# Kernel optimization log

Hardware: AMD Instinct MI355X
Metric: run time of the kernel (lower is better)

## Reference

```python
import jax, jax.numpy as jnp
import numpy as np

NEG = -1e9  # finite stand-in for log(0); keeps logsumexp/vjp NaN-free


def _hsmm_forward_loglik(log_B, log_pi, log_A, log_D):
    """Explicit-duration HSMM forward recursion in log-space for one sequence.

    log_B: (T, K) emission log-probs per state
    log_pi: (K,) initial state logits (log-normalized)
    log_A: (K, K) semi-Markov transition logits (NEG on diagonal, rows log-normalized)
    log_D: (K, Dmax) duration logits (rows log-normalized); column d <-> duration d+1
    Returns scalar log-likelihood log p(x_{1:T}).
    """
    T, K = log_B.shape
    Dmax = log_D.shape[1]
    # cB[t, j] = sum of emission log-probs of state j over first t steps; cB[0] = 0
    cB = jnp.concatenate([jnp.zeros((1, K), log_B.dtype), jnp.cumsum(log_B, axis=0)], axis=0)  # (T+1, K)
    log_Dt = log_D.T  # (Dmax, K), row d = duration d+1

    buf0 = jnp.full((Dmax, K), NEG, log_B.dtype)     # rolling buffer of start[t'] - cB[t']
    alpha0 = jnp.full((K,), NEG, log_B.dtype)

    def step(carry, t):
        buf, alpha_prev = carry
        # start[t, j]: log-prob a new segment starts at time t in state j
        trans = jax.scipy.special.logsumexp(alpha_prev[:, None] + log_A, axis=0)  # (K,)
        start = jnp.where(t == 0, log_pi, trans)
        buf = jnp.roll(buf, 1, axis=0).at[0].set(start - cB[t])
        # alpha[t, j] = cB[t+1, j] + lse_d ( start[t-d] - cB[t-d] + log_D[j, d] )
        alpha = cB[t + 1] + jax.scipy.special.logsumexp(buf + log_Dt, axis=0)  # (K,)
        return (buf, alpha), None
    (_, alpha_T), _ = jax.lax.scan(step, (buf0, alpha0), jnp.arange(T))
    return jax.scipy.special.logsumexp(alpha_T)


def setup_inputs() -> dict:
    key = jax.random.key(0)
    kB, kpi, kA, kD = jax.random.split(key, 4)
    B, T, K, Dmax = 32, 8192, 128, 128
    # emission log-probs (abstract emission pdf delegated to subclass -> model as input)
    log_B = jax.random.normal(kB, (B, T, K), dtype=jnp.float32) - 2.0
    log_pi = jax.nn.log_softmax(jax.random.normal(kpi, (K,), dtype=jnp.float32))
    # SEMI constraint: no self-transitions (diagonal = -inf), rows log-normalized
    A_raw = jax.random.normal(kA, (K, K), dtype=jnp.float32)
    A_raw = jnp.where(jnp.eye(K, dtype=bool), NEG, A_raw)
    log_A = jax.nn.log_softmax(A_raw, axis=1)
    log_D = jax.nn.log_softmax(jax.random.normal(kD, (K, Dmax), dtype=jnp.float32), axis=1)
    return {"log_B": log_B, "log_pi": log_pi, "log_A": log_A, "log_D": log_D}


def reference(log_B, log_pi, log_A, log_D):
    # Batched HSMM forward algorithm: per-sequence log-likelihoods, shape (B,)
    return jax.vmap(_hsmm_forward_loglik, in_axes=(0, None, None, None))(log_B, log_pi, log_A, log_D)
```

## Files before the change

kernel.cpp:

```cpp
#include <hip/hip_runtime.h>


typedef float f32x2 __attribute__((ext_vector_type(2)));

#define T_LEN 8192
#define KST   128
#define NTHR  512
#define SROW  160

__device__ __forceinline__ void barrier_nodrain() {
  asm volatile("s_waitcnt lgkmcnt(0)\n\ts_barrier" ::: "memory");
}

template <int CTRL>
__device__ __forceinline__ float dpp_mov(float x) {
  int y = __builtin_amdgcn_update_dpp(0, __builtin_bit_cast(int, x),
                                      CTRL, 0xF, 0xF, true);
  return __builtin_bit_cast(float, y);
}
template <int CTRL>
__device__ __forceinline__ f32x2 dpp_addv(f32x2 x) {
  f32x2 y;
  y.x = dpp_mov<CTRL>(x.x);
  y.y = dpp_mov<CTRL>(x.y);
  return x + y;
}

__device__ __forceinline__ void pk_fma(f32x2& d, f32x2 a, f32x2 b) {
  asm("v_pk_fma_f32 %0, %1, %2, %0" : "+v"(d) : "v"(a), "v"(b));
}
__device__ __forceinline__ void pk_fma_blo(f32x2& d, f32x2 a, f32x2 b) {
  asm("v_pk_fma_f32 %0, %1, %2, %0 op_sel:[0,0,0] op_sel_hi:[1,0,1]"
      : "+v"(d) : "v"(a), "v"(b));
}
__device__ __forceinline__ void pk_fma_bhi(f32x2& d, f32x2 a, f32x2 b) {
  asm("v_pk_fma_f32 %0, %1, %2, %0 op_sel:[0,1,0] op_sel_hi:[1,1,1]"
      : "+v"(d) : "v"(a), "v"(b));
}
__device__ __forceinline__ f32x2 pk_mul(f32x2 a, f32x2 b) {
  f32x2 d;
  asm("v_pk_mul_f32 %0, %1, %2" : "=v"(d) : "v"(a), "v"(b));
  return d;
}

template <int U>
__device__ __forceinline__ void step_body(
    int t0, int cc, int w, int L, int sel, int c2, int cc16,
    const float* __restrict__ pB0, const float* __restrict__ pB1,
    f32x2 (&qq)[16], const f32x2 (&Apl)[8], const f32x2 (&Aph)[8],
    f32x2 (&ee)[16], float (&lb0)[16], float (&lb1)[16],
    int& off,
    f32x2& psi, f32x2& invpsi, f32x2& exq, float& Ctot, f32x2& skeep,
    f32x2 expD0p, f32x2 pexpp, int swaddr,
    float* s_flat, float* m_sc, const float* ep_flat)
{
  const int t = t0 + U;
  const f32x2 expB = exq;

  int tn = t + 16; tn = (tn < T_LEN) ? tn : (T_LEN - 1);
  lb0[U] = pB0[(size_t)tn * KST];
  lb1[U] = pB1[(size_t)tn * KST];

  if (U == 15) {
    int rn = (t0 + 16 - cc16) & 127;
    int cl = (c2 + 4 * ((rn >> 4) & 7)) & 127;
    off = rn * 512 + cl * 4;
  } else {
    off = (off + 512) & 0xFFFF;
  }
  const f32x2 ne =
      *reinterpret_cast<const f32x2*>(reinterpret_cast<const char*>(ep_flat) + off);

  float Mp = m_sc[U & 1];

  const float* sp = s_flat + (U & 1) * SROW + 20 * cc;
  const float4 v0 = *(const float4*)(sp + 0),  v1 = *(const float4*)(sp + 4);
  const float4 v2 = *(const float4*)(sp + 8),  v3 = *(const float4*)(sp + 12);

  f32x2 da = pk_mul(qq[0], ee[(0 - U) & 15]);
  f32x2 db = pk_mul(qq[1], ee[(1 - U) & 15]);
#pragma unroll
  for (int k = 2; k < 16; k += 2) {
    pk_fma(da, qq[k],     ee[(k - U) & 15]);
    pk_fma(db, qq[k + 1], ee[(k + 1 - U) & 15]);
  }
  f32x2 dp = da + db;

  Mp = fminf(fmaxf(Mp, 1e-30f), 1e30f);
  const float rMp = __builtin_amdgcn_rcpf(Mp);
  Ctot += __logf(Mp);
  psi = pk_mul(psi, pk_mul(expB, f32x2{rMp, rMp}));

  f32x2 ma = {0.0f, 0.0f}, mb = {0.0f, 0.0f};
  pk_fma_blo(ma, Apl[0], f32x2{v0.x, v0.y});  pk_fma_bhi(mb, Aph[0], f32x2{v0.x, v0.y});
  pk_fma_blo(ma, Apl[1], f32x2{v0.z, v0.w});  pk_fma_bhi(mb, Aph[1], f32x2{v0.z, v0.w});
  pk_fma_blo(ma, Apl[2], f32x2{v1.x, v1.y});  pk_fma_bhi(mb, Aph[2], f32x2{v1.x, v1.y});
  pk_fma_blo(ma, Apl[3], f32x2{v1.z, v1.w});  pk_fma_bhi(mb, Aph[3], f32x2{v1.z, v1.w});
  pk_fma_blo(ma, Apl[4], f32x2{v2.x, v2.y});  pk_fma_bhi(mb, Aph[4], f32x2{v2.x, v2.y});
  pk_fma_blo(ma, Apl[5], f32x2{v2.z, v2.w});  pk_fma_bhi(mb, Aph[5], f32x2{v2.z, v2.w});
  pk_fma_blo(ma, Apl[6], f32x2{v3.x, v3.y});  pk_fma_bhi(mb, Aph[6], f32x2{v3.x, v3.y});
  pk_fma_blo(ma, Apl[7], f32x2{v3.z, v3.w});  pk_fma_bhi(mb, Aph[7], f32x2{v3.z, v3.w});
  f32x2 mp = ma + mb;

  dp = dpp_addv<0xB1>(dp); dp = dpp_addv<0x4E>(dp); dp = dpp_addv<0x141>(dp);
  mp = dpp_addv<0xB1>(mp); mp = dpp_addv<0x4E>(mp); mp = dpp_addv<0x141>(mp);

  f32x2 Qins = pk_mul(mp, invpsi);
  if (U == 0) { if (t0 == 0) Qins = pexpp; }
  f32x2 sacc = dp;
  pk_fma(sacc, Qins, expD0p);
  const f32x2 s = pk_mul(sacc, psi);

  exq.x = __expf(lb0[(U + 1) & 15]);
  exq.y = __expf(lb1[(U + 1) & 15]);

  if (sel == cc) qq[U] = Qins;

  if (w == 0) {
    float sm = fmaxf(s.x, s.y);
    sm = fmaxf(sm, dpp_mov<0x140>(sm));
    sm = fmaxf(sm, dpp_mov<0x142>(sm));
    sm = fmaxf(sm, dpp_mov<0x143>(sm));
    if (L == 63) m_sc[(U + 1) & 1] = sm;
  }

  if (cc == 0)
    *reinterpret_cast<f32x2*>(s_flat + ((U + 1) & 1) * SROW + swaddr) = s;

  ee[(15 - U) & 15] = ne;

  if (U == 15) {
#pragma unroll
    for (int k = 0; k < 16; ++k) qq[k] = pk_mul(qq[k], psi);
    psi = f32x2{1.0f, 1.0f};
  }
  invpsi.x = __builtin_amdgcn_rcpf(psi.x);
  invpsi.y = __builtin_amdgcn_rcpf(psi.y);

  skeep = s;
  barrier_nodrain();
}

__global__ __launch_bounds__(NTHR, 1) void hsmm_fwd_kernel(
    const float* __restrict__ logB_all,
    const float* __restrict__ logpi,
    const float* __restrict__ logA,
    const float* __restrict__ logD,
    float* __restrict__ out)
{
  const int tid = threadIdx.x;
  const int L   = tid & 63;
  const int w   = tid >> 6;
  const int cc  = L & 7;
  const int g   = L >> 3;
  const int j0  = 8 * w + g;
  const int j1  = j0 + 64;
  const int b   = blockIdx.x;
  const float* __restrict__ pB0 = logB_all + (size_t)b * T_LEN * KST + j0;
  const float* __restrict__ pB1 = pB0 + 64;

  __shared__ __align__(16) float epair[128 * 128];
  __shared__ __align__(16) float s_lds[2 * SROW];
  __shared__ float m_sc[2];
  __shared__ float fin[8];

  for (int idx = tid; idx < 128 * 128; idx += NTHR) {
    int d = idx >> 7, r = idx & 127;
    int j = r >> 1, hb = r & 1;
    int col = ((2 * j + 4 * ((d >> 4) & 7)) & 127) + hb;
    epair[(d << 7) + col] = (d == 0) ? 0.0f : __expf(logD[(j + 64 * hb) * 128 + d]);
  }
  if (tid < 2 * SROW) s_lds[tid] = 0.0f;
  if (tid < 2) m_sc[tid] = 1.0f;

  f32x2 Apl[8], Aph[8];
#pragma unroll
  for (int k = 0; k < 8; ++k) {
    int m = 8 * cc + k;
    Apl[k].x = __expf(logA[m * KST + j0]);
    Apl[k].y = __expf(logA[m * KST + j1]);
    Aph[k].x = __expf(logA[(m + 64) * KST + j0]);
    Aph[k].y = __expf(logA[(m + 64) * KST + j1]);
  }
  const f32x2 expD0p = {__expf(logD[j0 * 128]), __expf(logD[j1 * 128])};
  const f32x2 pexpp  = {__expf(logpi[j0]), __expf(logpi[j1])};
  const int   swaddr = 20 * w + 2 * g;
  const int   c2     = 16 * w + 2 * g;
  const int   cc16   = 16 * cc;

  f32x2 qq[16];
#pragma unroll
  for (int k = 0; k < 16; ++k) qq[k] = f32x2{0.0f, 0.0f};

  __syncthreads();

  f32x2 ee[16];
#pragma unroll
  for (int k = 0; k < 16; ++k) {
    int rA = (-(cc16 + k)) & 127;
    int cl = (c2 + 4 * ((rA >> 4) & 7)) & 127;
    ee[k] = *reinterpret_cast<const f32x2*>(&epair[(rA << 7) + cl]);
  }

  int off;
  {
    int r0 = (-cc16) & 127;
    int cl = (c2 + 4 * ((r0 >> 4) & 7)) & 127;
    off = r0 * 512 + cl * 4;
  }

  float lb0[16], lb1[16];
#pragma unroll
  for (int u = 0; u < 16; ++u) {
    lb0[u] = pB0[(size_t)u * KST];
    lb1[u] = pB1[(size_t)u * KST];
  }

  f32x2 psi = {1.0f, 1.0f}, invpsi = {1.0f, 1.0f};
  float Ctot = 0.0f;
  f32x2 skeep = {0.0f, 0.0f};
  f32x2 exq = {__expf(lb0[0]), __expf(lb1[0])};

#pragma unroll 1
  for (int t0 = 0; t0 < T_LEN; t0 += 16) {
    const int sel = (t0 >> 4) & 7;
#define STEP(U) step_body<U>(t0, cc, w, L, sel, c2, cc16, pB0, pB1, qq,       \
                             Apl, Aph, ee, lb0, lb1, off, psi, invpsi, exq,   \
                             Ctot, skeep, expD0p, pexpp, swaddr,              \
                             s_lds, m_sc, epair)
    STEP(0);  STEP(1);  STEP(2);  STEP(3);
    STEP(4);  STEP(5);  STEP(6);  STEP(7);
    STEP(8);  STEP(9);  STEP(10); STEP(11);
    STEP(12); STEP(13); STEP(14); STEP(15);
#undef STEP
  }

  float v = (cc == 0) ? (skeep.x + skeep.y) : 0.0f;
  v += __shfl_xor(v, 8);  v += __shfl_xor(v, 16); v += __shfl_xor(v, 32);
  if (L == 0) fin[w] = v;
  __syncthreads();
  if (tid == 0) {
    float tot = 0.0f;
#pragma unroll
    for (int i = 0; i < 8; ++i) tot += fin[i];
    out[b] = Ctot + __logf(tot);
  }
}

extern "C" void kernel_launch(void* const* d_in, const int* in_sizes, int n_in,
                              void* d_out, int out_size, void* d_ws, size_t ws_size,
                              hipStream_t stream) {
  const float* logB  = (const float*)d_in[0];
  const float* logpi = (const float*)d_in[1];
  const float* logA  = (const float*)d_in[2];
  const float* logD  = (const float*)d_in[3];
  float* out = (float*)d_out;
  const int B = out_size;
  hipLaunchKernelGGL(hsmm_fwd_kernel, dim3(B), dim3(NTHR), 0, stream,
                     logB, logpi, logA, logD, out);
}
```

Measured before the change: 4.098 ms.

## Precompute duration dot product for next step after barrier and pair adjacent states

Computes the duration-history dot product for step t+1 at the end of step t, so only the transition matvec and a single fused multiply-add remain on the serial path between barriers. The psi scaling is folded into a beta factor applied to the new segment term. Each thread now owns adjacent state pairs (2m, 2m+1), so emission log-probs load as one 64-bit load, and the A and D layouts are remapped to match. This shortens the per-step critical path but moves more work after the barrier and adds register pressure.

```diff
diff --git a/kernel.cpp b/kernel.cpp
--- a/kernel.cpp
+++ b/kernel.cpp
@@ -46,10 +46,10 @@
 template <int U>
 __device__ __forceinline__ void step_body(
     int t0, int cc, int w, int L, int sel, int c2, int cc16,
-    const float* __restrict__ pB0, const float* __restrict__ pB1,
+    const float* __restrict__ pB,
     f32x2 (&qq)[16], const f32x2 (&Apl)[8], const f32x2 (&Aph)[8],
-    f32x2 (&ee)[16], float (&lb0)[16], float (&lb1)[16],
-    int& off,
+    f32x2 (&ee)[16], f32x2 (&lbp)[16],
+    int& off, f32x2& dpc,
     f32x2& psi, f32x2& invpsi, f32x2& exq, float& Ctot, f32x2& skeep,
     f32x2 expD0p, f32x2 pexpp, int swaddr,
     float* s_flat, float* m_sc, const float* ep_flat)
@@ -57,10 +57,10 @@
   const int t = t0 + U;
   const f32x2 expB = exq;
 
-  int tn = t + 16; tn = (tn < T_LEN) ? tn : (T_LEN - 1);
-  lb0[U] = pB0[(size_t)tn * KST];
-  lb1[U] = pB1[(size_t)tn * KST];
-
+  const float* sp = s_flat + (U & 1) * SROW + 20 * cc;
+  const float4 v0 = *(const float4*)(sp + 0),  v1 = *(const float4*)(sp + 4);
+  const float4 v2 = *(const float4*)(sp + 8),  v3 = *(const float4*)(sp + 12);
+  float Mp = m_sc[U & 1];
   if (U == 15) {
     int rn = (t0 + 16 - cc16) & 127;
     int cl = (c2 + 4 * ((rn >> 4) & 7)) & 127;
@@ -70,26 +70,8 @@
   }
   const f32x2 ne =
       *reinterpret_cast<const f32x2*>(reinterpret_cast<const char*>(ep_flat) + off);
-
-  float Mp = m_sc[U & 1];
-
-  const float* sp = s_flat + (U & 1) * SROW + 20 * cc;
-  const float4 v0 = *(const float4*)(sp + 0),  v1 = *(const float4*)(sp + 4);
-  const float4 v2 = *(const float4*)(sp + 8),  v3 = *(const float4*)(sp + 12);
-
-  f32x2 da = pk_mul(qq[0], ee[(0 - U) & 15]);
-  f32x2 db = pk_mul(qq[1], ee[(1 - U) & 15]);
-#pragma unroll
-  for (int k = 2; k < 16; k += 2) {
-    pk_fma(da, qq[k],     ee[(k - U) & 15]);
-    pk_fma(db, qq[k + 1], ee[(k + 1 - U) & 15]);
-  }
-  f32x2 dp = da + db;
-
-  Mp = fminf(fmaxf(Mp, 1e-30f), 1e30f);
-  const float rMp = __builtin_amdgcn_rcpf(Mp);
-  Ctot += __logf(Mp);
-  psi = pk_mul(psi, pk_mul(expB, f32x2{rMp, rMp}));
+  int tn = t + 16; tn = (tn < T_LEN) ? tn : (T_LEN - 1);
+  lbp[U] = *reinterpret_cast<const f32x2*>(pB + (size_t)tn * KST);
 
   f32x2 ma = {0.0f, 0.0f}, mb = {0.0f, 0.0f};
   pk_fma_blo(ma, Apl[0], f32x2{v0.x, v0.y});  pk_fma_bhi(mb, Aph[0], f32x2{v0.x, v0.y});
@@ -102,19 +84,27 @@
   pk_fma_blo(ma, Apl[7], f32x2{v3.z, v3.w});  pk_fma_bhi(mb, Aph[7], f32x2{v3.z, v3.w});
   f32x2 mp = ma + mb;
 
-  dp = dpp_addv<0xB1>(dp); dp = dpp_addv<0x4E>(dp); dp = dpp_addv<0x141>(dp);
   mp = dpp_addv<0xB1>(mp); mp = dpp_addv<0x4E>(mp); mp = dpp_addv<0x141>(mp);
 
+  Mp = fminf(fmaxf(Mp, 1e-30f), 1e30f);
+  const float rMp = __builtin_amdgcn_rcpf(Mp);
+  Ctot += __logf(Mp);
+  const f32x2 er = pk_mul(expB, f32x2{rMp, rMp});
+  psi = pk_mul(psi, er);
+  const f32x2 beta = pk_mul(expD0p, er);
+
   f32x2 Qins = pk_mul(mp, invpsi);
-  if (U == 0) { if (t0 == 0) Qins = pexpp; }
-  f32x2 sacc = dp;
-  pk_fma(sacc, Qins, expD0p);
-  const f32x2 s = pk_mul(sacc, psi);
-
-  exq.x = __expf(lb0[(U + 1) & 15]);
-  exq.y = __expf(lb1[(U + 1) & 15]);
-
-  if (sel == cc) qq[U] = Qins;
+  f32x2 s = pk_mul(dpc, psi);
+  pk_fma(s, mp, beta);
+  if (U == 0) {
+    if (t0 == 0) {
+      Qins = pexpp;
+      s = pk_mul(pk_mul(pexpp, expD0p), psi);
+    }
+  }
+
+  if (cc == 0)
+    *reinterpret_cast<f32x2*>(s_flat + ((U + 1) & 1) * SROW + swaddr) = s;
 
   if (w == 0) {
     float sm = fmaxf(s.x, s.y);
@@ -124,10 +114,7 @@
     if (L == 63) m_sc[(U + 1) & 1] = sm;
   }
 
-  if (cc == 0)
-    *reinterpret_cast<f32x2*>(s_flat + ((U + 1) & 1) * SROW + swaddr) = s;
-
-  ee[(15 - U) & 15] = ne;
+  if (sel == cc) qq[U] = Qins;
 
   if (U == 15) {
 #pragma unroll
@@ -136,6 +123,21 @@
   }
   invpsi.x = __builtin_amdgcn_rcpf(psi.x);
   invpsi.y = __builtin_amdgcn_rcpf(psi.y);
+
+  ee[(15 - U) & 15] = ne;
+
+  f32x2 da = pk_mul(qq[0], ee[(0 - (U + 1)) & 15]);
+  f32x2 db = pk_mul(qq[1], ee[(1 - (U + 1)) & 15]);
+#pragma unroll
+  for (int k = 2; k < 16; k += 2) {
+    pk_fma(da, qq[k],     ee[(k - (U + 1)) & 15]);
+    pk_fma(db, qq[k + 1], ee[(k + 1 - (U + 1)) & 15]);
+  }
+  dpc = da + db;
+  dpc = dpp_addv<0xB1>(dpc); dpc = dpp_addv<0x4E>(dpc); dpc = dpp_addv<0x141>(dpc);
+
+  exq.x = __expf(lbp[(U + 1) & 15].x);
+  exq.y = __expf(lbp[(U + 1) & 15].y);
 
   skeep = s;
   barrier_nodrain();
@@ -153,11 +155,10 @@
   const int w   = tid >> 6;
   const int cc  = L & 7;
   const int g   = L >> 3;
-  const int j0  = 8 * w + g;
-  const int j1  = j0 + 64;
+  const int m   = 8 * w + g;
+  const int j0  = 2 * m;
   const int b   = blockIdx.x;
-  const float* __restrict__ pB0 = logB_all + (size_t)b * T_LEN * KST + j0;
-  const float* __restrict__ pB1 = pB0 + 64;
+  const float* __restrict__ pB = logB_all + (size_t)b * T_LEN * KST + j0;
 
   __shared__ __align__(16) float epair[128 * 128];
   __shared__ __align__(16) float s_lds[2 * SROW];
@@ -166,9 +167,9 @@
 
   for (int idx = tid; idx < 128 * 128; idx += NTHR) {
     int d = idx >> 7, r = idx & 127;
-    int j = r >> 1, hb = r & 1;
-    int col = ((2 * j + 4 * ((d >> 4) & 7)) & 127) + hb;
-    epair[(d << 7) + col] = (d == 0) ? 0.0f : __expf(logD[(j + 64 * hb) * 128 + d]);
+    int mm = r >> 1, hb = r & 1;
+    int col = ((2 * mm + 4 * ((d >> 4) & 7)) & 127) + hb;
+    epair[(d << 7) + col] = (d == 0) ? 0.0f : __expf(logD[(2 * mm + hb) * 128 + d]);
   }
   if (tid < 2 * SROW) s_lds[tid] = 0.0f;
   if (tid < 2) m_sc[tid] = 1.0f;
@@ -176,16 +177,16 @@
   f32x2 Apl[8], Aph[8];
 #pragma unroll
   for (int k = 0; k < 8; ++k) {
-    int m = 8 * cc + k;
-    Apl[k].x = __expf(logA[m * KST + j0]);
-    Apl[k].y = __expf(logA[m * KST + j1]);
-    Aph[k].x = __expf(logA[(m + 64) * KST + j0]);
-    Aph[k].y = __expf(logA[(m + 64) * KST + j1]);
-  }
-  const f32x2 expD0p = {__expf(logD[j0 * 128]), __expf(logD[j1 * 128])};
-  const f32x2 pexpp  = {__expf(logpi[j0]), __expf(logpi[j1])};
+    int se = 16 * cc + 2 * k;
+    Apl[k].x = __expf(logA[se * KST + j0]);
+    Apl[k].y = __expf(logA[se * KST + j0 + 1]);
+    Aph[k].x = __expf(logA[(se + 1) * KST + j0]);
+    Aph[k].y = __expf(logA[(se + 1) * KST + j0 + 1]);
+  }
+  const f32x2 expD0p = {__expf(logD[j0 * 128]), __expf(logD[(j0 + 1) * 128])};
+  const f32x2 pexpp  = {__expf(logpi[j0]), __expf(logpi[j0 + 1])};
   const int   swaddr = 20 * w + 2 * g;
-  const int   c2     = 16 * w + 2 * g;
+  const int   c2     = 2 * m;
   const int   cc16   = 16 * cc;
 
   f32x2 qq[16];
@@ -209,25 +210,23 @@
     off = r0 * 512 + cl * 4;
   }
 
-  float lb0[16], lb1[16];
-#pragma unroll
-  for (int u = 0; u < 16; ++u) {
-    lb0[u] = pB0[(size_t)u * KST];
-    lb1[u] = pB1[(size_t)u * KST];
-  }
+  f32x2 lbp[16];
+#pragma unroll
+  for (int u = 0; u < 16; ++u)
+    lbp[u] = *reinterpret_cast<const f32x2*>(pB + (size_t)u * KST);
 
   f32x2 psi = {1.0f, 1.0f}, invpsi = {1.0f, 1.0f};
+  f32x2 dpc = {0.0f, 0.0f};
   float Ctot = 0.0f;
   f32x2 skeep = {0.0f, 0.0f};
-  f32x2 exq = {__expf(lb0[0]), __expf(lb1[0])};
+  f32x2 exq = {__expf(lbp[0].x), __expf(lbp[0].y)};
 
 #pragma unroll 1
   for (int t0 = 0; t0 < T_LEN; t0 += 16) {
     const int sel = (t0 >> 4) & 7;
-#define STEP(U) step_body<U>(t0, cc, w, L, sel, c2, cc16, pB0, pB1, qq,       \
-                             Apl, Aph, ee, lb0, lb1, off, psi, invpsi, exq,   \
-                             Ctot, skeep, expD0p, pexpp, swaddr,              \
-                             s_lds, m_sc, epair)
+#define STEP(U) step_body<U>(t0, cc, w, L, sel, c2, cc16, pB, qq, Apl, Aph,   \
+                             ee, lbp, off, dpc, psi, invpsi, exq, Ctot,       \
+                             skeep, expD0p, pexpp, swaddr, s_lds, m_sc, epair)
     STEP(0);  STEP(1);  STEP(2);  STEP(3);
     STEP(4);  STEP(5);  STEP(6);  STEP(7);
     STEP(8);  STEP(9);  STEP(10); STEP(11);
```

After: 5.002 ms. 1.22x slower.

## Pack exchanged alpha values as bf16 and delay max-rescaling by one step

Applied to the files above, without the earlier changes.

The per-step alpha vector shared through LDS is now packed to bf16 pairs, which halves LDS write and read traffic. Each step's scaling factor comes from a max that is two steps old, stored in a 4-slot ring, and is applied as a reciprocal square root so each factor's log is split across two steps. The LDS reads are hoisted to the start of the step body and the exp/qq updates are moved after the store. The trade-off is lower precision in the transition matvec, which may hurt accuracy, and a more complex rescaling scheme whose numerical stability depends on the delayed max.

```diff
diff --git a/kernel.cpp b/kernel.cpp
--- a/kernel.cpp
+++ b/kernel.cpp
@@ -2,11 +2,12 @@
 
 
 typedef float f32x2 __attribute__((ext_vector_type(2)));
+typedef unsigned int u32x4 __attribute__((ext_vector_type(4)));
 
 #define T_LEN 8192
 #define KST   128
 #define NTHR  512
-#define SROW  160
+#define SROWU 96
 
 __device__ __forceinline__ void barrier_nodrain() {
   asm volatile("s_waitcnt lgkmcnt(0)\n\ts_barrier" ::: "memory");
@@ -41,6 +42,12 @@
   f32x2 d;
   asm("v_pk_mul_f32 %0, %1, %2" : "=v"(d) : "v"(a), "v"(b));
   return d;
+}
+__device__ __forceinline__ f32x2 bf2(unsigned int u) {
+  f32x2 r;
+  r.x = __builtin_bit_cast(float, u << 16);
+  r.y = __builtin_bit_cast(float, u & 0xFFFF0000u);
+  return r;
 }
 
 template <int U>
@@ -52,7 +59,7 @@
     int& off,
     f32x2& psi, f32x2& invpsi, f32x2& exq, float& Ctot, f32x2& skeep,
     f32x2 expD0p, f32x2 pexpp, int swaddr,
-    float* s_flat, float* m_sc, const float* ep_flat)
+    unsigned int* s_flat, float* m_sc, const float* ep_flat)
 {
   const int t = t0 + U;
   const f32x2 expB = exq;
@@ -60,6 +67,12 @@
   int tn = t + 16; tn = (tn < T_LEN) ? tn : (T_LEN - 1);
   lb0[U] = pB0[(size_t)tn * KST];
   lb1[U] = pB1[(size_t)tn * KST];
+
+  float Mp = m_sc[U & 3];
+
+  const unsigned int* sp = s_flat + (U & 1) * SROWU + 12 * cc;
+  const u32x4 q0 = *(const u32x4*)(sp + 0);
+  const u32x4 q1 = *(const u32x4*)(sp + 4);
 
   if (U == 15) {
     int rn = (t0 + 16 - cc16) & 127;
@@ -71,12 +84,6 @@
   const f32x2 ne =
       *reinterpret_cast<const f32x2*>(reinterpret_cast<const char*>(ep_flat) + off);
 
-  float Mp = m_sc[U & 1];
-
-  const float* sp = s_flat + (U & 1) * SROW + 20 * cc;
-  const float4 v0 = *(const float4*)(sp + 0),  v1 = *(const float4*)(sp + 4);
-  const float4 v2 = *(const float4*)(sp + 8),  v3 = *(const float4*)(sp + 12);
-
   f32x2 da = pk_mul(qq[0], ee[(0 - U) & 15]);
   f32x2 db = pk_mul(qq[1], ee[(1 - U) & 15]);
 #pragma unroll
@@ -87,19 +94,20 @@
   f32x2 dp = da + db;
 
   Mp = fminf(fmaxf(Mp, 1e-30f), 1e30f);
-  const float rMp = __builtin_amdgcn_rcpf(Mp);
-  Ctot += __logf(Mp);
-  psi = pk_mul(psi, pk_mul(expB, f32x2{rMp, rMp}));
+  const float rMp = __builtin_amdgcn_rsqf(Mp);
+  Ctot += 0.5f * __logf(Mp);
+  const f32x2 rv = {rMp, rMp};
+  psi = pk_mul(psi, pk_mul(expB, rv));
 
   f32x2 ma = {0.0f, 0.0f}, mb = {0.0f, 0.0f};
-  pk_fma_blo(ma, Apl[0], f32x2{v0.x, v0.y});  pk_fma_bhi(mb, Aph[0], f32x2{v0.x, v0.y});
-  pk_fma_blo(ma, Apl[1], f32x2{v0.z, v0.w});  pk_fma_bhi(mb, Aph[1], f32x2{v0.z, v0.w});
-  pk_fma_blo(ma, Apl[2], f32x2{v1.x, v1.y});  pk_fma_bhi(mb, Aph[2], f32x2{v1.x, v1.y});
-  pk_fma_blo(ma, Apl[3], f32x2{v1.z, v1.w});  pk_fma_bhi(mb, Aph[3], f32x2{v1.z, v1.w});
-  pk_fma_blo(ma, Apl[4], f32x2{v2.x, v2.y});  pk_fma_bhi(mb, Aph[4], f32x2{v2.x, v2.y});
-  pk_fma_blo(ma, Apl[5], f32x2{v2.z, v2.w});  pk_fma_bhi(mb, Aph[5], f32x2{v2.z, v2.w});
-  pk_fma_blo(ma, Apl[6], f32x2{v3.x, v3.y});  pk_fma_bhi(mb, Aph[6], f32x2{v3.x, v3.y});
-  pk_fma_blo(ma, Apl[7], f32x2{v3.z, v3.w});  pk_fma_bhi(mb, Aph[7], f32x2{v3.z, v3.w});
+  { f32x2 vp = bf2(q0.x); pk_fma_blo(ma, Apl[0], vp); pk_fma_bhi(mb, Aph[0], vp); }
+  { f32x2 vp = bf2(q0.y); pk_fma_blo(ma, Apl[1], vp); pk_fma_bhi(mb, Aph[1], vp); }
+  { f32x2 vp = bf2(q0.z); pk_fma_blo(ma, Apl[2], vp); pk_fma_bhi(mb, Aph[2], vp); }
+  { f32x2 vp = bf2(q0.w); pk_fma_blo(ma, Apl[3], vp); pk_fma_bhi(mb, Aph[3], vp); }
+  { f32x2 vp = bf2(q1.x); pk_fma_blo(ma, Apl[4], vp); pk_fma_bhi(mb, Aph[4], vp); }
+  { f32x2 vp = bf2(q1.y); pk_fma_blo(ma, Apl[5], vp); pk_fma_bhi(mb, Aph[5], vp); }
+  { f32x2 vp = bf2(q1.z); pk_fma_blo(ma, Apl[6], vp); pk_fma_bhi(mb, Aph[6], vp); }
+  { f32x2 vp = bf2(q1.w); pk_fma_blo(ma, Apl[7], vp); pk_fma_bhi(mb, Aph[7], vp); }
   f32x2 mp = ma + mb;
 
   dp = dpp_addv<0xB1>(dp); dp = dpp_addv<0x4E>(dp); dp = dpp_addv<0x141>(dp);
@@ -111,21 +119,24 @@
   pk_fma(sacc, Qins, expD0p);
   const f32x2 s = pk_mul(sacc, psi);
 
-  exq.x = __expf(lb0[(U + 1) & 15]);
-  exq.y = __expf(lb1[(U + 1) & 15]);
-
-  if (sel == cc) qq[U] = Qins;
+  if (cc == 0) {
+    unsigned int pk;
+    asm("v_cvt_pk_bf16_f32 %0, %1, %2" : "=v"(pk) : "v"(s.x), "v"(s.y));
+    s_flat[((U + 1) & 1) * SROWU + swaddr] = pk;
+  }
 
   if (w == 0) {
     float sm = fmaxf(s.x, s.y);
     sm = fmaxf(sm, dpp_mov<0x140>(sm));
     sm = fmaxf(sm, dpp_mov<0x142>(sm));
     sm = fmaxf(sm, dpp_mov<0x143>(sm));
-    if (L == 63) m_sc[(U + 1) & 1] = sm;
-  }
-
-  if (cc == 0)
-    *reinterpret_cast<f32x2*>(s_flat + ((U + 1) & 1) * SROW + swaddr) = s;
+    if (L == 63) m_sc[(U + 2) & 3] = sm;
+  }
+
+  exq.x = __expf(lb0[(U + 1) & 15]);
+  exq.y = __expf(lb1[(U + 1) & 15]);
+
+  if (sel == cc) qq[U] = Qins;
 
   ee[(15 - U) & 15] = ne;
 
@@ -160,8 +171,8 @@
   const float* __restrict__ pB1 = pB0 + 64;
 
   __shared__ __align__(16) float epair[128 * 128];
-  __shared__ __align__(16) float s_lds[2 * SROW];
-  __shared__ float m_sc[2];
+  __shared__ __align__(16) unsigned int s_lds[2 * SROWU];
+  __shared__ float m_sc[4];
   __shared__ float fin[8];
 
   for (int idx = tid; idx < 128 * 128; idx += NTHR) {
@@ -170,8 +181,8 @@
     int col = ((2 * j + 4 * ((d >> 4) & 7)) & 127) + hb;
     epair[(d << 7) + col] = (d == 0) ? 0.0f : __expf(logD[(j + 64 * hb) * 128 + d]);
   }
-  if (tid < 2 * SROW) s_lds[tid] = 0.0f;
-  if (tid < 2) m_sc[tid] = 1.0f;
+  if (tid < 2 * SROWU) s_lds[tid] = 0u;
+  if (tid < 4) m_sc[tid] = 1.0f;
 
   f32x2 Apl[8], Aph[8];
 #pragma unroll
@@ -184,7 +195,7 @@
   }
   const f32x2 expD0p = {__expf(logD[j0 * 128]), __expf(logD[j1 * 128])};
   const f32x2 pexpp  = {__expf(logpi[j0]), __expf(logpi[j1])};
-  const int   swaddr = 20 * w + 2 * g;
+  const int   swaddr = 12 * w + g;
   const int   c2     = 16 * w + 2 * g;
   const int   cc16   = 16 * cc;
 
```

Result: slower. 4.396 ms (+7.3%).
